# Optimization experiments

Measured on AMD Instinct MI355X. Metric: run time of the kernel, lower is better.

## Reference

```python
import jax, jax.numpy as jnp
import numpy as np

EMBED_DIM = 768
HEADS = 8
HEAD_DIM = 128  # gnn_hidden_dim
OUT_DIM = HEADS * HEAD_DIM  # 1024, concat=True
NEG_SLOPE = 0.2  # PyG GATConv leaky_relu slope


def setup_inputs() -> dict:
    key = jax.random.key(0)
    ks = jax.random.split(key, 12)
    N, E = 10000, 160000
    x = jax.random.normal(ks[0], (N, EMBED_DIM), dtype=jnp.float32)
    edge_index = jax.random.randint(ks[1], (2, E), 0, N, dtype=jnp.int32)
    edge_attr = jax.random.uniform(ks[2], (E, 1), dtype=jnp.float32)
    # GATConv params (single layer, edge_dim=1)
    sc = 1.0 / np.sqrt(EMBED_DIM)
    W = jax.random.normal(ks[3], (EMBED_DIM, OUT_DIM), dtype=jnp.float32) * sc
    att_src = jax.random.normal(ks[4], (HEADS, HEAD_DIM), dtype=jnp.float32) * 0.1
    att_dst = jax.random.normal(ks[5], (HEADS, HEAD_DIM), dtype=jnp.float32) * 0.1
    W_edge = jax.random.normal(ks[6], (1, OUT_DIM), dtype=jnp.float32)
    att_edge = jax.random.normal(ks[7], (HEADS, HEAD_DIM), dtype=jnp.float32) * 0.1
    bias = jnp.zeros((OUT_DIM,), dtype=jnp.float32)
    # final classifier: in = 3*OUT_DIM (global pool + text node + image node)
    clf_W = jax.random.normal(ks[8], (3 * OUT_DIM, 2), dtype=jnp.float32) * (1.0 / np.sqrt(3 * OUT_DIM))
    clf_b = jnp.zeros((2,), dtype=jnp.float32)
    return {
        'x': x, 'edge_index': edge_index, 'edge_attr': edge_attr,
        'text_idx': 0, 'image_idx': 1,
        'W': W, 'att_src': att_src, 'att_dst': att_dst,
        'W_edge': W_edge, 'att_edge': att_edge, 'bias': bias,
        'clf_W': clf_W, 'clf_b': clf_b,
    }


def gat_layer(x, edge_index, edge_attr, W, att_src, att_dst, W_edge, att_edge, bias):
    N = x.shape[0]
    # add self-loops with edge_attr = mean of existing edge_attr (PyG default fill_value='mean')
    loop = jnp.arange(N, dtype=edge_index.dtype)
    ei = jnp.concatenate([edge_index, jnp.stack([loop, loop])], axis=1)
    ea_mean = jnp.mean(edge_attr, axis=0, keepdims=True)
    ea = jnp.concatenate([edge_attr, jnp.broadcast_to(ea_mean, (N, edge_attr.shape[1]))], axis=0)
    src, dst = ei[0], ei[1]
    xs = (x @ W).reshape(N, HEADS, HEAD_DIM)             # [N, H, C]
    a_src = jnp.einsum('nhc,hc->nh', xs, att_src)        # per-node src logits
    a_dst = jnp.einsum('nhc,hc->nh', xs, att_dst)
    e_emb = (ea @ W_edge).reshape(-1, HEADS, HEAD_DIM)   # [Etot, H, C]
    a_edge = jnp.einsum('ehc,hc->eh', e_emb, att_edge)
    alpha = jax.nn.leaky_relu(a_src[src] + a_dst[dst] + a_edge, NEG_SLOPE)  # [Etot, H]
    # softmax over incoming edges of each dst node
    m = jax.ops.segment_max(alpha, dst, num_segments=N)
    ex = jnp.exp(alpha - m[dst])
    denom = jax.ops.segment_sum(ex, dst, num_segments=N)
    w = ex / denom[dst]                                  # normalized attention [Etot, H]
    msg = xs[src] * w[:, :, None]                        # [Etot, H, C]
    out = jax.ops.segment_sum(msg, dst, num_segments=N)  # [N, H, C]
    return out.reshape(N, OUT_DIM) + bias


def reference(x, edge_index, edge_attr, text_idx, image_idx,
              W, att_src, att_dst, W_edge, att_edge, bias, clf_W, clf_b):
    # single GAT layer (num_gat_layers=1 -> no ELU/dropout after, eval mode)
    h = gat_layer(x, edge_index, edge_attr, W, att_src, att_dst, W_edge, att_edge, bias)
    g = jnp.mean(h, axis=0, keepdims=True)               # global_mean_pool, batch=None
    t = h[text_idx][None, :]
    im = h[image_idx][None, :]
    fused = jnp.concatenate([g, t, im], axis=1)          # [1, 3*OUT_DIM]
    logits = fused @ clf_W + clf_b                       # [1, 2]
    return logits
```

## Files before the change

### kernel.cpp

```cpp
#include <hip/hip_runtime.h>

#define NN 10000
#define EE 160000
#define ETOT (EE + NN)
#define EMB 768
#define ODIM 1024
#define NEG 0.2f
#define CAP 56

#define OFF_P      0
#define OFF_Q      12288
#define OFF_EAACC  12296
#define OFF_CNTD   12304
#define OFF_CNTS   22304
#define ZERO_START 12296
#define ZERO_CNT   20008
#define OFF_A      32304
#define OFF_SRCD   192304
#define OFF_DSTS   752304
#define OFF_PACK   1312304
#define OFF_EXD    1482304
#define OFF_EXS    5962304
#define OFF_RDEN   10442304
#define OFF_S      10522304
#define OFF_Z      10602304
#define OFF_YPART  10614592

__global__ __launch_bounds__(256) void k1f(
    const float* __restrict__ W, const float* __restrict__ att_src,
    const float* __restrict__ att_dst, const float* __restrict__ W_edge,
    const float* __restrict__ att_edge, const float* __restrict__ edge_attr,
    const int* __restrict__ ei, float* __restrict__ ws) {
  int b = blockIdx.x;
  if (b < 48) {
    int tid = b * 256 + threadIdx.x;
    int k = tid >> 4, j = tid & 15, h = j & 7;
    const float* att = (j < 8) ? att_src : att_dst;
    const float* wp = W + k * ODIM + h * 128;
    const float* ap = att + h * 128;
    float acc = 0.f;
    #pragma unroll 8
    for (int c = 0; c < 128; ++c) acc += wp[c] * ap[c];
    ws[OFF_P + k * 16 + j] = acc;
  } else if (b == 48) {
    if (threadIdx.x < 8) {
      int h = threadIdx.x;
      float acc = 0.f;
      #pragma unroll 8
      for (int c = 0; c < 128; ++c) acc += W_edge[h * 128 + c] * att_edge[h * 128 + c];
      ws[OFF_Q + h] = acc;
    }
  } else if (b < 113) {
    int bi = b - 49;
    float acc = 0.f;
    for (int i = bi * 256 + threadIdx.x; i < EE; i += 64 * 256) acc += edge_attr[i];
    #pragma unroll
    for (int off = 32; off > 0; off >>= 1) acc += __shfl_down(acc, off, 64);
    if ((threadIdx.x & 63) == 0) atomicAdd(&ws[OFF_EAACC], acc);
  } else {
    int e = (b - 113) * 256 + threadIdx.x;
    if (e >= ETOT) return;
    int src, dst;
    if (e < EE) { src = ei[e]; dst = ei[EE + e]; } else { src = dst = e - EE; }
    int* cntd = (int*)(ws + OFF_CNTD);
    int* cnts = (int*)(ws + OFF_CNTS);
    int pd = atomicAdd(&cntd[dst], 1);
    if (pd < CAP) ((int*)(ws + OFF_SRCD))[dst * CAP + pd] = src;
    int ps = atomicAdd(&cnts[src], 1);
    if (ps < CAP) ((int*)(ws + OFF_DSTS))[src * CAP + ps] = dst;
    if (pd > CAP) pd = CAP;
    if (ps > CAP) ps = CAP;
    ((int*)(ws + OFF_PACK))[e] = pd | (ps << 16);
  }
}

__global__ __launch_bounds__(256) void kAx(const float* __restrict__ x,
                                           float* __restrict__ ws) {
  __shared__ float smem[12288];
  for (int i = threadIdx.x; i < 3072; i += 256)
    ((float4*)smem)[i] = ((const float4*)(ws + OFF_P))[i];
  __syncthreads();
  int nl = threadIdx.x & 31, cg = threadIdx.x >> 5;
  int n = blockIdx.x * 32 + nl;
  float a[16];
  #pragma unroll
  for (int j = 0; j < 16; ++j) a[j] = 0.f;
  if (n < NN) {
    const float4* xr = (const float4*)(x + n * EMB + cg * 96);
    for (int kk = 0; kk < 24; ++kk) {
      float4 xv = xr[kk];
      const float* pr = &smem[(cg * 96 + kk * 4) * 16];
      #pragma unroll
      for (int j = 0; j < 16; ++j) a[j] += xv.x * pr[j];
      #pragma unroll
      for (int j = 0; j < 16; ++j) a[j] += xv.y * pr[16 + j];
      #pragma unroll
      for (int j = 0; j < 16; ++j) a[j] += xv.z * pr[32 + j];
      #pragma unroll
      for (int j = 0; j < 16; ++j) a[j] += xv.w * pr[48 + j];
    }
  }
  __syncthreads();
  #pragma unroll
  for (int j = 0; j < 16; ++j) smem[(cg * 16 + j) * 33 + nl] = a[j];
  __syncthreads();
  for (int w = threadIdx.x; w < 512; w += 256) {
    int rnl = w >> 4, j = w & 15;
    int nn = blockIdx.x * 32 + rnl;
    if (nn < NN) {
      float s = 0.f;
      #pragma unroll
      for (int c2 = 0; c2 < 8; ++c2) s += smem[(c2 * 16 + j) * 33 + rnl];
      ws[OFF_A + nn * 16 + j] = s;
    }
  }
}

__global__ __launch_bounds__(128) void kE(const int* __restrict__ ei,
                                          const float* __restrict__ edge_attr,
                                          const float* __restrict__ bias,
                                          const float* __restrict__ clf_W,
                                          const float* __restrict__ clf_b,
                                          float* __restrict__ out,
                                          float* __restrict__ ws) {
  __shared__ float red[4];
  int* wsI = (int*)ws;
  if (blockIdx.x < 1329) {
    int e = blockIdx.x * 128 + threadIdx.x;
    if (e >= ETOT) return;
    int src, dst; float ea;
    if (e < EE) { src = ei[e]; dst = ei[EE + e]; ea = edge_attr[e]; }
    else { src = dst = e - EE; ea = ws[OFF_EAACC] * (1.0f / EE); }
    int pk = wsI[OFF_PACK + e];
    int pd = pk & 0xffff, ps = pk >> 16;
    const float4* as4 = (const float4*)(ws + OFF_A + src * 16);
    const float4* ad4 = (const float4*)(ws + OFF_A + dst * 16 + 8);
    float4 s0 = as4[0], s1 = as4[1], d0 = ad4[0], d1 = ad4[1];
    float asr[8] = {s0.x, s0.y, s0.z, s0.w, s1.x, s1.y, s1.z, s1.w};
    float ads[8] = {d0.x, d0.y, d0.z, d0.w, d1.x, d1.y, d1.z, d1.w};
    float ex[8];
    #pragma unroll
    for (int h = 0; h < 8; ++h) {
      float v = asr[h] + ads[h] + ea * ws[OFF_Q + h];
      v = (v >= 0.f) ? v : NEG * v;
      ex[h] = __expf(v);
    }
    float4 e0 = make_float4(ex[0], ex[1], ex[2], ex[3]);
    float4 e1 = make_float4(ex[4], ex[5], ex[6], ex[7]);
    if (pd < CAP) {
      float4* p = (float4*)(ws + OFF_EXD + (dst * CAP + pd) * 8);
      p[0] = e0; p[1] = e1;
    }
    if (ps < CAP) {
      float4* p = (float4*)(ws + OFF_EXS + (src * CAP + ps) * 8);
      p[0] = e0; p[1] = e1;
    }
  } else {
    int t = threadIdx.x;
    float b0 = 0.f, b1 = 0.f;
    for (int i = t; i < 3072; i += 128) {
      float f = bias[i & 1023];
      b0 += f * clf_W[2 * i];
      b1 += f * clf_W[2 * i + 1];
    }
    #pragma unroll
    for (int o = 32; o > 0; o >>= 1) {
      b0 += __shfl_down(b0, o, 64);
      b1 += __shfl_down(b1, o, 64);
    }
    if ((t & 63) == 0) { red[(t >> 6) * 2] = b0; red[(t >> 6) * 2 + 1] = b1; }
    __syncthreads();
    if (t == 0) {
      out[0] = clf_b[0] + red[0] + red[2];
      out[1] = clf_b[1] + red[1] + red[3];
    }
  }
}

__global__ __launch_bounds__(128) void kD(float* __restrict__ ws) {
  int t = blockIdx.x * 128 + threadIdx.x;
  int dst = t >> 3, h = t & 7;
  int deg = ((const int*)(ws + OFF_CNTD))[dst];
  if (deg > CAP) deg = CAP;
  const float* base = ws + OFF_EXD + dst * (CAP * 8) + h;
  float den = 0.f;
  for (int j = 0; j < deg; ++j) den += base[j * 8];
  ws[OFF_RDEN + t] = 1.0f / den;
}

__global__ __launch_bounds__(128) void kSZ(const float* __restrict__ x,
                                           const int* __restrict__ tptr,
                                           const int* __restrict__ iptr,
                                           float* __restrict__ ws) {
  __shared__ float sm[512];
  if (blockIdx.x < 625) {
    int t = blockIdx.x * 128 + threadIdx.x;
    int src = t >> 3, h = t & 7;
    int deg = ((const int*)(ws + OFF_CNTS))[src];
    if (deg > CAP) deg = CAP;
    const int* dstrow = (const int*)(ws + OFF_DSTS) + src * CAP;
    const float* exrow = ws + OFF_EXS + src * (CAP * 8) + h;
    float s = 0.f;
    for (int j = 0; j < deg; ++j)
      s += exrow[j * 8] * ws[OFF_RDEN + dstrow[j] * 8 + h];
    ws[OFF_S + t] = s;
  } else {
    float* wL = sm;
    int* srcS = (int*)(sm + 448);
    int* degP = (int*)(sm + 508);
    int r = blockIdx.x - 625;
    int d = r / 6, kc = r % 6;
    int target = (d == 0) ? tptr[0] : iptr[0];
    if (threadIdx.x == 0) {
      int dg = ((const int*)(ws + OFF_CNTD))[target];
      degP[0] = (dg > CAP) ? CAP : dg;
    }
    __syncthreads();
    int deg = degP[0];
    for (int idx = threadIdx.x; idx < deg * 8; idx += 128) {
      int j = idx >> 3, h = idx & 7;
      wL[idx] = ws[OFF_EXD + (target * CAP + j) * 8 + h]
              * ws[OFF_RDEN + target * 8 + h];
      if (h == 0) srcS[j] = ((const int*)(ws + OFF_SRCD))[target * CAP + j];
    }
    __syncthreads();
    int col = kc * 128 + threadIdx.x;
    float acc[8];
    #pragma unroll
    for (int h = 0; h < 8; ++h) acc[h] = 0.f;
    for (int j = 0; j < deg; ++j) {
      float xv = x[srcS[j] * EMB + col];
      const float* wv = &wL[j * 8];
      #pragma unroll
      for (int h = 0; h < 8; ++h) acc[h] += wv[h] * xv;
    }
    #pragma unroll
    for (int h = 0; h < 8; ++h) ws[OFF_Z + (d * 8 + h) * EMB + col] = acc[h];
  }
}

__global__ __launch_bounds__(256) void k7s(const float* __restrict__ x,
                                           float* __restrict__ ws) {
  __shared__ float sL[64 * 8];
  int base = blockIdx.x * 64;
  int c = blockIdx.y;
  for (int i = threadIdx.x; i < 512; i += 256) {
    int n = base + (i >> 3);
    sL[i] = (n < NN) ? ws[OFF_S + base * 8 + i] : 0.f;
  }
  __syncthreads();
  int col = c * 256 + threadIdx.x;
  float acc[8];
  #pragma unroll
  for (int h = 0; h < 8; ++h) acc[h] = 0.f;
  int nmax = (NN - base < 64) ? (NN - base) : 64;
  for (int i = 0; i < nmax; ++i) {
    float xv = x[(base + i) * EMB + col];
    const float* sv = &sL[i * 8];
    #pragma unroll
    for (int h = 0; h < 8; ++h) acc[h] += xv * sv[h];
  }
  float* yp = ws + OFF_YPART + blockIdx.x * 6144 + col;
  #pragma unroll
  for (int h = 0; h < 8; ++h) yp[h * 768] = acc[h];
}

__global__ __launch_bounds__(128) void k8(const float* __restrict__ W,
                                          const float* __restrict__ clf_W,
                                          float* __restrict__ out,
                                          float* __restrict__ ws) {
  __shared__ float vL[144];
  __shared__ float red[4];
  int h = blockIdx.x, kc = blockIdx.y, kbase = kc * 48;
  for (int i = threadIdx.x; i < 144; i += 128) {
    int d = i / 48, k = i - d * 48;
    float v;
    if (d == 0) {
      float acc = 0.f;
      for (int b = 0; b < 157; ++b)
        acc += ws[OFF_YPART + b * 6144 + h * 768 + kbase + k];
      v = acc * (1.0f / NN);
    } else {
      v = ws[OFF_Z + ((d - 1) * 8 + h) * 768 + kbase + k];
    }
    vL[i] = v;
  }
  __syncthreads();
  int c = threadIdx.x;
  float a0 = 0.f, a1 = 0.f, a2 = 0.f;
  #pragma unroll 4
  for (int k = 0; k < 48; ++k) {
    float wv = W[(kbase + k) * ODIM + h * 128 + c];
    a0 += vL[k] * wv;
    a1 += vL[48 + k] * wv;
    a2 += vL[96 + k] * wv;
  }
  int ib = h * 128 + c;
  float l0 = a0 * clf_W[2 * ib] + a1 * clf_W[2 * (1024 + ib)]
           + a2 * clf_W[2 * (2048 + ib)];
  float l1 = a0 * clf_W[2 * ib + 1] + a1 * clf_W[2 * (1024 + ib) + 1]
           + a2 * clf_W[2 * (2048 + ib) + 1];
  #pragma unroll
  for (int o = 32; o > 0; o >>= 1) {
    l0 += __shfl_down(l0, o, 64);
    l1 += __shfl_down(l1, o, 64);
  }
  if ((threadIdx.x & 63) == 0) {
    red[(threadIdx.x >> 6) * 2] = l0;
    red[(threadIdx.x >> 6) * 2 + 1] = l1;
  }
  __syncthreads();
  if (threadIdx.x == 0) {
    atomicAdd(&out[0], red[0] + red[2]);
    atomicAdd(&out[1], red[1] + red[3]);
  }
}

extern "C" void kernel_launch(void* const* d_in, const int* in_sizes, int n_in,
                              void* d_out, int out_size, void* d_ws, size_t ws_size,
                              hipStream_t stream) {
  const float* x        = (const float*)d_in[0];
  const int*   ei       = (const int*)d_in[1];
  const float* edge_attr= (const float*)d_in[2];
  const int*   tptr     = (const int*)d_in[3];
  const int*   iptr     = (const int*)d_in[4];
  const float* W        = (const float*)d_in[5];
  const float* att_src  = (const float*)d_in[6];
  const float* att_dst  = (const float*)d_in[7];
  const float* W_edge   = (const float*)d_in[8];
  const float* att_edge = (const float*)d_in[9];
  const float* bias     = (const float*)d_in[10];
  const float* clf_W    = (const float*)d_in[11];
  const float* clf_b    = (const float*)d_in[12];
  float* ws  = (float*)d_ws;
  float* out = (float*)d_out;

  hipMemsetAsync(ws + ZERO_START, 0, ZERO_CNT * sizeof(float), stream);
  k1f<<<778, 256, 0, stream>>>(W, att_src, att_dst, W_edge, att_edge, edge_attr, ei, ws);
  kAx<<<313, 256, 0, stream>>>(x, ws);
  kE<<<1330, 128, 0, stream>>>(ei, edge_attr, bias, clf_W, clf_b, out, ws);
  kD<<<625, 128, 0, stream>>>(ws);
  kSZ<<<637, 128, 0, stream>>>(x, tptr, iptr, ws);
  dim3 g7(157, 3);
  k7s<<<g7, 256, 0, stream>>>(x, ws);
  dim3 g8(8, 16);
  k8<<<g8, 128, 0, stream>>>(W, clf_W, out, ws);
}
```

Measured before the change: 192.7 us.

## Store edge exps once by edge id; restructure kAx with transposed projection

Edge exponentials are now written once per edge into a flat array, and the CSR-like buckets hold (edge id, neighbor) pairs. This replaces the two duplicated per-bucket exp copies and the packed slot array. kD and kSZ gather exps indirectly through the edge id. kAx now uses a transposed projection matrix with 16 nodes per block and coalesced x reads. The bias/classifier init moves into k1f. The indirect gathers in the reduction kernels may lose locality in exchange for fewer writes and a smaller workspace.

```diff
diff --git a/kernel.cpp b/kernel.cpp
--- a/kernel.cpp
+++ b/kernel.cpp
@@ -8,7 +8,7 @@
 #define NEG 0.2f
 #define CAP 56
 
-#define OFF_P      0
+#define OFF_PT     0
 #define OFF_Q      12288
 #define OFF_EAACC  12296
 #define OFF_CNTD   12304
@@ -16,22 +16,24 @@
 #define ZERO_START 12296
 #define ZERO_CNT   20008
 #define OFF_A      32304
-#define OFF_SRCD   192304
-#define OFF_DSTS   752304
-#define OFF_PACK   1312304
-#define OFF_EXD    1482304
-#define OFF_EXS    5962304
-#define OFF_RDEN   10442304
-#define OFF_S      10522304
-#define OFF_Z      10602304
-#define OFF_YPART  10614592
+#define OFF_EDD    192304
+#define OFF_EDS    1312304
+#define OFF_EX     2432304
+#define OFF_RDEN   3792304
+#define OFF_S      3872304
+#define OFF_Z      3952304
+#define OFF_YPART  3964592
 
 __global__ __launch_bounds__(256) void k1f(
     const float* __restrict__ W, const float* __restrict__ att_src,
     const float* __restrict__ att_dst, const float* __restrict__ W_edge,
     const float* __restrict__ att_edge, const float* __restrict__ edge_attr,
-    const int* __restrict__ ei, float* __restrict__ ws) {
+    const int* __restrict__ ei, const float* __restrict__ bias,
+    const float* __restrict__ clf_W, const float* __restrict__ clf_b,
+    float* __restrict__ out, float* __restrict__ ws) {
+  __shared__ float red[8];
   int b = blockIdx.x;
+  int* wsI = (int*)ws;
   if (b < 48) {
     int tid = b * 256 + threadIdx.x;
     int k = tid >> 4, j = tid & 15, h = j & 7;
@@ -41,7 +43,7 @@
     float acc = 0.f;
     #pragma unroll 8
     for (int c = 0; c < 128; ++c) acc += wp[c] * ap[c];
-    ws[OFF_P + k * 16 + j] = acc;
+    ws[OFF_PT + j * 768 + k] = acc;
   } else if (b == 48) {
     if (threadIdx.x < 8) {
       int h = threadIdx.x;
@@ -57,108 +59,19 @@
     #pragma unroll
     for (int off = 32; off > 0; off >>= 1) acc += __shfl_down(acc, off, 64);
     if ((threadIdx.x & 63) == 0) atomicAdd(&ws[OFF_EAACC], acc);
-  } else {
+  } else if (b < 778) {
     int e = (b - 113) * 256 + threadIdx.x;
     if (e >= ETOT) return;
     int src, dst;
     if (e < EE) { src = ei[e]; dst = ei[EE + e]; } else { src = dst = e - EE; }
-    int* cntd = (int*)(ws + OFF_CNTD);
-    int* cnts = (int*)(ws + OFF_CNTS);
-    int pd = atomicAdd(&cntd[dst], 1);
-    if (pd < CAP) ((int*)(ws + OFF_SRCD))[dst * CAP + pd] = src;
-    int ps = atomicAdd(&cnts[src], 1);
-    if (ps < CAP) ((int*)(ws + OFF_DSTS))[src * CAP + ps] = dst;
-    if (pd > CAP) pd = CAP;
-    if (ps > CAP) ps = CAP;
-    ((int*)(ws + OFF_PACK))[e] = pd | (ps << 16);
-  }
-}
-
-__global__ __launch_bounds__(256) void kAx(const float* __restrict__ x,
-                                           float* __restrict__ ws) {
-  __shared__ float smem[12288];
-  for (int i = threadIdx.x; i < 3072; i += 256)
-    ((float4*)smem)[i] = ((const float4*)(ws + OFF_P))[i];
-  __syncthreads();
-  int nl = threadIdx.x & 31, cg = threadIdx.x >> 5;
-  int n = blockIdx.x * 32 + nl;
-  float a[16];
-  #pragma unroll
-  for (int j = 0; j < 16; ++j) a[j] = 0.f;
-  if (n < NN) {
-    const float4* xr = (const float4*)(x + n * EMB + cg * 96);
-    for (int kk = 0; kk < 24; ++kk) {
-      float4 xv = xr[kk];
-      const float* pr = &smem[(cg * 96 + kk * 4) * 16];
-      #pragma unroll
-      for (int j = 0; j < 16; ++j) a[j] += xv.x * pr[j];
-      #pragma unroll
-      for (int j = 0; j < 16; ++j) a[j] += xv.y * pr[16 + j];
-      #pragma unroll
-      for (int j = 0; j < 16; ++j) a[j] += xv.z * pr[32 + j];
-      #pragma unroll
-      for (int j = 0; j < 16; ++j) a[j] += xv.w * pr[48 + j];
-    }
-  }
-  __syncthreads();
-  #pragma unroll
-  for (int j = 0; j < 16; ++j) smem[(cg * 16 + j) * 33 + nl] = a[j];
-  __syncthreads();
-  for (int w = threadIdx.x; w < 512; w += 256) {
-    int rnl = w >> 4, j = w & 15;
-    int nn = blockIdx.x * 32 + rnl;
-    if (nn < NN) {
-      float s = 0.f;
-      #pragma unroll
-      for (int c2 = 0; c2 < 8; ++c2) s += smem[(c2 * 16 + j) * 33 + rnl];
-      ws[OFF_A + nn * 16 + j] = s;
-    }
-  }
-}
-
-__global__ __launch_bounds__(128) void kE(const int* __restrict__ ei,
-                                          const float* __restrict__ edge_attr,
-                                          const float* __restrict__ bias,
-                                          const float* __restrict__ clf_W,
-                                          const float* __restrict__ clf_b,
-                                          float* __restrict__ out,
-                                          float* __restrict__ ws) {
-  __shared__ float red[4];
-  int* wsI = (int*)ws;
-  if (blockIdx.x < 1329) {
-    int e = blockIdx.x * 128 + threadIdx.x;
-    if (e >= ETOT) return;
-    int src, dst; float ea;
-    if (e < EE) { src = ei[e]; dst = ei[EE + e]; ea = edge_attr[e]; }
-    else { src = dst = e - EE; ea = ws[OFF_EAACC] * (1.0f / EE); }
-    int pk = wsI[OFF_PACK + e];
-    int pd = pk & 0xffff, ps = pk >> 16;
-    const float4* as4 = (const float4*)(ws + OFF_A + src * 16);
-    const float4* ad4 = (const float4*)(ws + OFF_A + dst * 16 + 8);
-    float4 s0 = as4[0], s1 = as4[1], d0 = ad4[0], d1 = ad4[1];
-    float asr[8] = {s0.x, s0.y, s0.z, s0.w, s1.x, s1.y, s1.z, s1.w};
-    float ads[8] = {d0.x, d0.y, d0.z, d0.w, d1.x, d1.y, d1.z, d1.w};
-    float ex[8];
-    #pragma unroll
-    for (int h = 0; h < 8; ++h) {
-      float v = asr[h] + ads[h] + ea * ws[OFF_Q + h];
-      v = (v >= 0.f) ? v : NEG * v;
-      ex[h] = __expf(v);
-    }
-    float4 e0 = make_float4(ex[0], ex[1], ex[2], ex[3]);
-    float4 e1 = make_float4(ex[4], ex[5], ex[6], ex[7]);
-    if (pd < CAP) {
-      float4* p = (float4*)(ws + OFF_EXD + (dst * CAP + pd) * 8);
-      p[0] = e0; p[1] = e1;
-    }
-    if (ps < CAP) {
-      float4* p = (float4*)(ws + OFF_EXS + (src * CAP + ps) * 8);
-      p[0] = e0; p[1] = e1;
-    }
+    int pd = atomicAdd(&wsI[OFF_CNTD + dst], 1);
+    if (pd < CAP) ((int2*)(wsI + OFF_EDD))[dst * CAP + pd] = make_int2(e, src);
+    int ps = atomicAdd(&wsI[OFF_CNTS + src], 1);
+    if (ps < CAP) ((int2*)(wsI + OFF_EDS))[src * CAP + ps] = make_int2(e, dst);
   } else {
     int t = threadIdx.x;
     float b0 = 0.f, b1 = 0.f;
-    for (int i = t; i < 3072; i += 128) {
+    for (int i = t; i < 3072; i += 256) {
       float f = bias[i & 1023];
       b0 += f * clf_W[2 * i];
       b1 += f * clf_W[2 * i + 1];
@@ -171,20 +84,78 @@
     if ((t & 63) == 0) { red[(t >> 6) * 2] = b0; red[(t >> 6) * 2 + 1] = b1; }
     __syncthreads();
     if (t == 0) {
-      out[0] = clf_b[0] + red[0] + red[2];
-      out[1] = clf_b[1] + red[1] + red[3];
-    }
-  }
+      out[0] = clf_b[0] + red[0] + red[2] + red[4] + red[6];
+      out[1] = clf_b[1] + red[1] + red[3] + red[5] + red[7];
+    }
+  }
+}
+
+__global__ __launch_bounds__(256) void kAx(const float* __restrict__ x,
+                                           float* __restrict__ ws) {
+  __shared__ float sm[12288];
+  for (int i = threadIdx.x; i < 3072; i += 256)
+    ((float4*)sm)[i] = ((const float4*)(ws + OFF_PT))[i];
+  __syncthreads();
+  int li = threadIdx.x & 15, nl = threadIdx.x >> 4;
+  int n = blockIdx.x * 16 + nl;
+  float a[16];
+  #pragma unroll
+  for (int j = 0; j < 16; ++j) a[j] = 0.f;
+  const float4* xr = (const float4*)(x + n * EMB);
+  const float4* pT4 = (const float4*)sm;
+  for (int i = 0; i < 12; ++i) {
+    float4 xv = xr[li + i * 16];
+    int k4 = li + i * 16;
+    #pragma unroll
+    for (int j = 0; j < 16; ++j) {
+      float4 p = pT4[j * 192 + k4];
+      a[j] += xv.x * p.x + xv.y * p.y + xv.z * p.z + xv.w * p.w;
+    }
+  }
+  __syncthreads();
+  #pragma unroll
+  for (int j = 0; j < 16; ++j) sm[threadIdx.x * 17 + j] = a[j];
+  __syncthreads();
+  int rn = threadIdx.x >> 4, rj = threadIdx.x & 15;
+  float s = 0.f;
+  #pragma unroll
+  for (int c = 0; c < 16; ++c) s += sm[(rn * 16 + c) * 17 + rj];
+  ws[OFF_A + (blockIdx.x * 16 + rn) * 16 + rj] = s;
+}
+
+__global__ __launch_bounds__(256) void kE(const int* __restrict__ ei,
+                                          const float* __restrict__ edge_attr,
+                                          float* __restrict__ ws) {
+  int e = blockIdx.x * 256 + threadIdx.x;
+  if (e >= ETOT) return;
+  int src, dst; float ea;
+  if (e < EE) { src = ei[e]; dst = ei[EE + e]; ea = edge_attr[e]; }
+  else { src = dst = e - EE; ea = ws[OFF_EAACC] * (1.0f / EE); }
+  const float4* as4 = (const float4*)(ws + OFF_A + src * 16);
+  const float4* ad4 = (const float4*)(ws + OFF_A + dst * 16 + 8);
+  float4 s0 = as4[0], s1 = as4[1], d0 = ad4[0], d1 = ad4[1];
+  float asr[8] = {s0.x, s0.y, s0.z, s0.w, s1.x, s1.y, s1.z, s1.w};
+  float ads[8] = {d0.x, d0.y, d0.z, d0.w, d1.x, d1.y, d1.z, d1.w};
+  float ex[8];
+  #pragma unroll
+  for (int h = 0; h < 8; ++h) {
+    float v = asr[h] + ads[h] + ea * ws[OFF_Q + h];
+    v = (v >= 0.f) ? v : NEG * v;
+    ex[h] = __expf(v);
+  }
+  float4* p = (float4*)(ws + OFF_EX + e * 8);
+  p[0] = make_float4(ex[0], ex[1], ex[2], ex[3]);
+  p[1] = make_float4(ex[4], ex[5], ex[6], ex[7]);
 }
 
 __global__ __launch_bounds__(128) void kD(float* __restrict__ ws) {
   int t = blockIdx.x * 128 + threadIdx.x;
   int dst = t >> 3, h = t & 7;
-  int deg = ((const int*)(ws + OFF_CNTD))[dst];
-  if (deg > CAP) deg = CAP;
-  const float* base = ws + OFF_EXD + dst * (CAP * 8) + h;
+  const int* wsI = (const int*)ws;
+  int deg = wsI[OFF_CNTD + dst]; if (deg > CAP) deg = CAP;
+  const int2* edd = (const int2*)(wsI + OFF_EDD) + dst * CAP;
   float den = 0.f;
-  for (int j = 0; j < deg; ++j) den += base[j * 8];
+  for (int j = 0; j < deg; ++j) den += ws[OFF_EX + edd[j].x * 8 + h];
   ws[OFF_RDEN + t] = 1.0f / den;
 }
 
@@ -193,16 +164,17 @@
                                            const int* __restrict__ iptr,
                                            float* __restrict__ ws) {
   __shared__ float sm[512];
+  const int* wsI = (const int*)ws;
   if (blockIdx.x < 625) {
     int t = blockIdx.x * 128 + threadIdx.x;
     int src = t >> 3, h = t & 7;
-    int deg = ((const int*)(ws + OFF_CNTS))[src];
-    if (deg > CAP) deg = CAP;
-    const int* dstrow = (const int*)(ws + OFF_DSTS) + src * CAP;
-    const float* exrow = ws + OFF_EXS + src * (CAP * 8) + h;
+    int deg = wsI[OFF_CNTS + src]; if (deg > CAP) deg = CAP;
+    const int2* eds = (const int2*)(wsI + OFF_EDS) + src * CAP;
     float s = 0.f;
-    for (int j = 0; j < deg; ++j)
-      s += exrow[j * 8] * ws[OFF_RDEN + dstrow[j] * 8 + h];
+    for (int j = 0; j < deg; ++j) {
+      int2 ed = eds[j];
+      s += ws[OFF_EX + ed.x * 8 + h] * ws[OFF_RDEN + ed.y * 8 + h];
+    }
     ws[OFF_S + t] = s;
   } else {
     float* wL = sm;
@@ -212,16 +184,16 @@
     int d = r / 6, kc = r % 6;
     int target = (d == 0) ? tptr[0] : iptr[0];
     if (threadIdx.x == 0) {
-      int dg = ((const int*)(ws + OFF_CNTD))[target];
+      int dg = wsI[OFF_CNTD + target];
       degP[0] = (dg > CAP) ? CAP : dg;
     }
     __syncthreads();
     int deg = degP[0];
     for (int idx = threadIdx.x; idx < deg * 8; idx += 128) {
       int j = idx >> 3, h = idx & 7;
-      wL[idx] = ws[OFF_EXD + (target * CAP + j) * 8 + h]
-              * ws[OFF_RDEN + target * 8 + h];
-      if (h == 0) srcS[j] = ((const int*)(ws + OFF_SRCD))[target * CAP + j];
+      int2 ed = ((const int2*)(wsI + OFF_EDD))[target * CAP + j];
+      wL[idx] = ws[OFF_EX + ed.x * 8 + h] * ws[OFF_RDEN + target * 8 + h];
+      if (h == 0) srcS[j] = ed.y;
     }
     __syncthreads();
     int col = kc * 128 + threadIdx.x;
@@ -336,9 +308,10 @@
   float* out = (float*)d_out;
 
   hipMemsetAsync(ws + ZERO_START, 0, ZERO_CNT * sizeof(float), stream);
-  k1f<<<778, 256, 0, stream>>>(W, att_src, att_dst, W_edge, att_edge, edge_attr, ei, ws);
-  kAx<<<313, 256, 0, stream>>>(x, ws);
-  kE<<<1330, 128, 0, stream>>>(ei, edge_attr, bias, clf_W, clf_b, out, ws);
+  k1f<<<779, 256, 0, stream>>>(W, att_src, att_dst, W_edge, att_edge, edge_attr,
+                               ei, bias, clf_W, clf_b, out, ws);
+  kAx<<<625, 256, 0, stream>>>(x, ws);
+  kE<<<665, 256, 0, stream>>>(ei, edge_attr, ws);
   kD<<<625, 128, 0, stream>>>(ws);
   kSZ<<<637, 128, 0, stream>>>(x, tptr, iptr, ws);
   dim3 g7(157, 3);
```

After: 195.2 us. Within noise of the previous version (+1.3%).
